# Kernel optimization log

Hardware: AMD Instinct MI355X
Metric: run time of the kernel (lower is better)

## Reference

```python
import jax, jax.numpy as jnp
import numpy as np

EPS = 1e-10


def setup_inputs() -> dict:
    key = jax.random.key(0)
    k1, k2 = jax.random.split(key)
    supports = jax.random.normal(k1, (32, 512, 1024), dtype=jnp.float32)
    targets = jax.random.normal(k2, (32, 512, 1024), dtype=jnp.float32)
    return {"supports": supports, "targets": targets}


def reference(supports, targets):
    # targets: [B, T, D], supports: [B, S, D] -> sim: [B, T, S]
    # F.cosine_similarity(a, b, eps): dot / max(||a||*||b||, eps)
    dots = jnp.einsum("btd,bsd->bts", targets, supports)
    t_norm = jnp.linalg.norm(targets, axis=-1)   # [B, T]
    s_norm = jnp.linalg.norm(supports, axis=-1)  # [B, S]
    denom = jnp.maximum(t_norm[:, :, None] * s_norm[:, None, :], EPS)
    sim = dots / denom
    # normalize=True default: map (-1, 1) -> (0, 1)
    return (sim + 1.0) * 0.5
```

## Files before the change

kernel.cpp:

```cpp
#include <hip/hip_runtime.h>
#include <hip/hip_bf16.h>

typedef __attribute__((ext_vector_type(8))) short short8;
typedef __attribute__((ext_vector_type(4))) float f32x4;

#define NBATCH 32
#define NT 512
#define NS 512
#define ND 1024
#define BM 128
#define BN 128
#define BK 32
#define NK (ND / BK)

__device__ __forceinline__ short f2bf(float f) {
    union { __hip_bfloat16 h; short s; } u;
    u.h = __float2bfloat16(f);
    return u.s;
}

__device__ __forceinline__ short8 cvt8(float4 a, float4 b) {
    short8 r;
    r[0] = f2bf(a.x); r[1] = f2bf(a.y); r[2] = f2bf(a.z); r[3] = f2bf(a.w);
    r[4] = f2bf(b.x); r[5] = f2bf(b.y); r[6] = f2bf(b.z); r[7] = f2bf(b.w);
    return r;
}

__device__ __forceinline__ float ssq4(float s, float4 a) {
    return fmaf(a.x, a.x, fmaf(a.y, a.y, fmaf(a.z, a.z, fmaf(a.w, a.w, s))));
}

__global__ __launch_bounds__(512, 4)
void paircos_mfma(const float* __restrict__ sup, const float* __restrict__ tgt,
                  float* __restrict__ out) {
    __shared__ __align__(16) short As[2][BM * BK];
    __shared__ __align__(16) short Bs[2][BN * BK];
    __shared__ float tn[BM];
    __shared__ float sn[BN];

    const int tid = threadIdx.x;
    const int l    = blockIdx.x;
    const int wgid = (l & 7) * 64 + (l >> 3);
    const int b    = wgid >> 4;
    const int til  = wgid & 15;
    const int bt0  = (til >> 2) * BM;
    const int bs0  = (til & 3) * BN;

    const int seg  = tid & 3;
    const int srow = tid >> 2;

    const float* gA = tgt + (size_t)b * NT * ND + (size_t)(bt0 + srow) * ND + seg * 8;
    const float* gB = sup + (size_t)b * NS * ND + (size_t)(bs0 + srow) * ND + seg * 8;

    const int wave = tid >> 6;
    const int lane = tid & 63;
    const int wr  = (wave >> 2) * 64;
    const int wc  = (wave & 3) * 32;
    const int lhi = lane >> 4;
    const int llo = lane & 15;

    f32x4 acc[4][2];
#pragma unroll
    for (int m = 0; m < 4; ++m)
#pragma unroll
        for (int n = 0; n < 2; ++n)
            acc[m][n] = (f32x4){0.f, 0.f, 0.f, 0.f};

    float sqa = 0.f, sqb = 0.f;

    float4 eA0, eA1, eB0, eB1, oA0, oA1, oB0, oB1;

    const int offw = srow * BK + (((seg + (srow >> 1)) & 3) * 8);

#define LOADT(A0, A1, B0, B1, KK)                                              \
    do {                                                                       \
        A0 = *reinterpret_cast<const float4*>(gA + (KK) * BK);                 \
        A1 = *reinterpret_cast<const float4*>(gA + (KK) * BK + 4);             \
        B0 = *reinterpret_cast<const float4*>(gB + (KK) * BK);                 \
        B1 = *reinterpret_cast<const float4*>(gB + (KK) * BK + 4);             \
    } while (0)

#define STORET(A0, A1, B0, B1, P)                                              \
    do {                                                                       \
        sqa = ssq4(ssq4(sqa, A0), A1);                                         \
        *reinterpret_cast<short8*>(&As[P][offw]) = cvt8(A0, A1);               \
        sqb = ssq4(ssq4(sqb, B0), B1);                                         \
        *reinterpret_cast<short8*>(&Bs[P][offw]) = cvt8(B0, B1);               \
    } while (0)

#define FRAG_READ(P)                                                           \
    do {                                                                       \
        _Pragma("unroll") for (int m = 0; m < 4; ++m) {                        \
            const int row = wr + m * 16 + llo;                                 \
            const int off = row * BK + (((lhi + (row >> 1)) & 3) * 8);         \
            af[m] = *reinterpret_cast<const short8*>(&As[P][off]);             \
        }                                                                      \
        _Pragma("unroll") for (int n = 0; n < 2; ++n) {                        \
            const int row = wc + n * 16 + llo;                                 \
            const int off = row * BK + (((lhi + (row >> 1)) & 3) * 8);         \
            bfr[n] = *reinterpret_cast<const short8*>(&Bs[P][off]);            \
        }                                                                      \
    } while (0)

#define MFMA_BLOCK()                                                           \
    do {                                                                       \
        __builtin_amdgcn_s_setprio(1);                                         \
        _Pragma("unroll") for (int m = 0; m < 4; ++m)                          \
            _Pragma("unroll") for (int n = 0; n < 2; ++n)                      \
                acc[m][n] = __builtin_amdgcn_mfma_f32_16x16x32_bf16(           \
                    af[m], bfr[n], acc[m][n], 0, 0, 0);                        \
        __builtin_amdgcn_s_setprio(0);                                         \
    } while (0)

#define PHASE_FENCE()                                                          \
    do {                                                                       \
        asm volatile("s_waitcnt lgkmcnt(0)" ::: "memory");                     \
        __builtin_amdgcn_s_barrier();                                          \
        asm volatile("" ::: "memory");                                         \
    } while (0)

    LOADT(eA0, eA1, eB0, eB1, 0);
    STORET(eA0, eA1, eB0, eB1, 0);
    LOADT(eA0, eA1, eB0, eB1, 1);
    LOADT(oA0, oA1, oB0, oB1, 2);
    PHASE_FENCE();

    for (int k = 0; k < NK; k += 2) {
        {
            short8 af[4], bfr[2];
            FRAG_READ(0);
            STORET(eA0, eA1, eB0, eB1, 1);
            if (k + 3 < NK) LOADT(eA0, eA1, eB0, eB1, k + 3);
            MFMA_BLOCK();
            PHASE_FENCE();
        }
        {
            short8 af[4], bfr[2];
            FRAG_READ(1);
            if (k + 2 < NK) STORET(oA0, oA1, oB0, oB1, 0);
            if (k + 4 < NK) LOADT(oA0, oA1, oB0, oB1, k + 4);
            MFMA_BLOCK();
            PHASE_FENCE();
        }
    }

    sqa += __shfl_xor(sqa, 1);
    sqa += __shfl_xor(sqa, 2);
    sqb += __shfl_xor(sqb, 1);
    sqb += __shfl_xor(sqb, 2);
    if (seg == 0) {
        tn[srow] = sqrtf(sqa);
        sn[srow] = sqrtf(sqb);
    }
    __syncthreads();

    float* outp = out + (size_t)b * NT * NS;
#pragma unroll
    for (int m = 0; m < 4; ++m) {
        const int lr0 = wr + m * 16 + lhi * 4;
#pragma unroll
        for (int n = 0; n < 2; ++n) {
            const int lc = wc + n * 16 + llo;
            const float snv = sn[lc];
            const int col = bs0 + lc;
#pragma unroll
            for (int j = 0; j < 4; ++j) {
                const float denom = fmaxf(tn[lr0 + j] * snv, 1e-10f);
                outp[(size_t)(bt0 + lr0 + j) * NS + col] =
                    acc[m][n][j] / denom * 0.5f + 0.5f;
            }
        }
    }
}

extern "C" void kernel_launch(void* const* d_in, const int* in_sizes, int n_in,
                              void* d_out, int out_size, void* d_ws, size_t ws_size,
                              hipStream_t stream) {
    const float* sup = (const float*)d_in[0];
    const float* tgt = (const float*)d_in[1];
    float* out = (float*)d_out;
    (void)in_sizes; (void)n_in; (void)out_size; (void)d_ws; (void)ws_size;
    paircos_mfma<<<dim3(16 * NBATCH), 512, 0, stream>>>(sup, tgt, out);
}
```

Measured before the change: 39.30 us.

## Double K tile to 64 with XOR LDS swizzle and fewer barriers

Raises the K tile from 32 to 64 so each barrier-separated phase does two MFMA blocks, halving the number of LDS barriers per output tile. Each thread now loads two rows (row and row+64) with 8 segments per row. The LDS layout switches to an XOR swizzle to avoid bank conflicts, and the prefetch depth drops from two tiles in registers to one. This doubles the LDS footprint and changes the register pressure and latency-hiding balance.

```diff
diff --git a/kernel.cpp b/kernel.cpp
--- a/kernel.cpp
+++ b/kernel.cpp
@@ -10,7 +10,7 @@
 #define ND 1024
 #define BM 128
 #define BN 128
-#define BK 32
+#define BK 64
 #define NK (ND / BK)
 
 __device__ __forceinline__ short f2bf(float f) {
@@ -46,8 +46,8 @@
     const int bt0  = (til >> 2) * BM;
     const int bs0  = (til & 3) * BN;
 
-    const int seg  = tid & 3;
-    const int srow = tid >> 2;
+    const int seg  = tid & 7;
+    const int srow = tid >> 3;
 
     const float* gA = tgt + (size_t)b * NT * ND + (size_t)(bt0 + srow) * ND + seg * 8;
     const float* gB = sup + (size_t)b * NS * ND + (size_t)(bs0 + srow) * ND + seg * 8;
@@ -66,38 +66,48 @@
         for (int n = 0; n < 2; ++n)
             acc[m][n] = (f32x4){0.f, 0.f, 0.f, 0.f};
 
-    float sqa = 0.f, sqb = 0.f;
+    float sqa0 = 0.f, sqa1 = 0.f, sqb0 = 0.f, sqb1 = 0.f;
 
-    float4 eA0, eA1, eB0, eB1, oA0, oA1, oB0, oB1;
+    float4 pA0, pA1, pA2, pA3, pB0, pB1, pB2, pB3;
 
-    const int offw = srow * BK + (((seg + (srow >> 1)) & 3) * 8);
+    const int pu   = (seg ^ (srow & 7)) * 8;
+    const int offw0 = srow * BK + pu;
+    const int offw1 = (srow + 64) * BK + pu;
 
-#define LOADT(A0, A1, B0, B1, KK)                                              \
+#define LOADT(KK)                                                              \
     do {                                                                       \
-        A0 = *reinterpret_cast<const float4*>(gA + (KK) * BK);                 \
-        A1 = *reinterpret_cast<const float4*>(gA + (KK) * BK + 4);             \
-        B0 = *reinterpret_cast<const float4*>(gB + (KK) * BK);                 \
-        B1 = *reinterpret_cast<const float4*>(gB + (KK) * BK + 4);             \
+        pA0 = *reinterpret_cast<const float4*>(gA + (KK) * BK);                \
+        pA1 = *reinterpret_cast<const float4*>(gA + (KK) * BK + 4);            \
+        pA2 = *reinterpret_cast<const float4*>(gA + (KK) * BK + 64 * ND);      \
+        pA3 = *reinterpret_cast<const float4*>(gA + (KK) * BK + 64 * ND + 4);  \
+        pB0 = *reinterpret_cast<const float4*>(gB + (KK) * BK);                \
+        pB1 = *reinterpret_cast<const float4*>(gB + (KK) * BK + 4);            \
+        pB2 = *reinterpret_cast<const float4*>(gB + (KK) * BK + 64 * ND);      \
+        pB3 = *reinterpret_cast<const float4*>(gB + (KK) * BK + 64 * ND + 4);  \
     } while (0)
 
-#define STORET(A0, A1, B0, B1, P)                                              \
+#define STORET(P)                                                              \
     do {                                                                       \
-        sqa = ssq4(ssq4(sqa, A0), A1);                                         \
-        *reinterpret_cast<short8*>(&As[P][offw]) = cvt8(A0, A1);               \
-        sqb = ssq4(ssq4(sqb, B0), B1);                                         \
-        *reinterpret_cast<short8*>(&Bs[P][offw]) = cvt8(B0, B1);               \
+        sqa0 = ssq4(ssq4(sqa0, pA0), pA1);                                     \
+        *reinterpret_cast<short8*>(&As[P][offw0]) = cvt8(pA0, pA1);            \
+        sqa1 = ssq4(ssq4(sqa1, pA2), pA3);                                     \
+        *reinterpret_cast<short8*>(&As[P][offw1]) = cvt8(pA2, pA3);            \
+        sqb0 = ssq4(ssq4(sqb0, pB0), pB1);                                     \
+        *reinterpret_cast<short8*>(&Bs[P][offw0]) = cvt8(pB0, pB1);            \
+        sqb1 = ssq4(ssq4(sqb1, pB2), pB3);                                     \
+        *reinterpret_cast<short8*>(&Bs[P][offw1]) = cvt8(pB2, pB3);            \
     } while (0)
 
-#define FRAG_READ(P)                                                           \
+#define FRAG_READ(P, KS)                                                       \
     do {                                                                       \
         _Pragma("unroll") for (int m = 0; m < 4; ++m) {                        \
             const int row = wr + m * 16 + llo;                                 \
-            const int off = row * BK + (((lhi + (row >> 1)) & 3) * 8);         \
+            const int off = row * BK + ((((KS) * 4 + lhi) ^ (row & 7)) * 8);   \
             af[m] = *reinterpret_cast<const short8*>(&As[P][off]);             \
         }                                                                      \
         _Pragma("unroll") for (int n = 0; n < 2; ++n) {                        \
             const int row = wc + n * 16 + llo;                                 \
-            const int off = row * BK + (((lhi + (row >> 1)) & 3) * 8);         \
+            const int off = row * BK + ((((KS) * 4 + lhi) ^ (row & 7)) * 8);   \
             bfr[n] = *reinterpret_cast<const short8*>(&Bs[P][off]);            \
         }                                                                      \
     } while (0)
@@ -119,38 +129,35 @@
         asm volatile("" ::: "memory");                                         \
     } while (0)
 
-    LOADT(eA0, eA1, eB0, eB1, 0);
-    STORET(eA0, eA1, eB0, eB1, 0);
-    LOADT(eA0, eA1, eB0, eB1, 1);
-    LOADT(oA0, oA1, oB0, oB1, 2);
+    LOADT(0);
+    STORET(0);
+    LOADT(1);
     PHASE_FENCE();
 
-    for (int k = 0; k < NK; k += 2) {
-        {
-            short8 af[4], bfr[2];
-            FRAG_READ(0);
-            STORET(eA0, eA1, eB0, eB1, 1);
-            if (k + 3 < NK) LOADT(eA0, eA1, eB0, eB1, k + 3);
-            MFMA_BLOCK();
-            PHASE_FENCE();
-        }
-        {
-            short8 af[4], bfr[2];
-            FRAG_READ(1);
-            if (k + 2 < NK) STORET(oA0, oA1, oB0, oB1, 0);
-            if (k + 4 < NK) LOADT(oA0, oA1, oB0, oB1, k + 4);
-            MFMA_BLOCK();
-            PHASE_FENCE();
-        }
+    for (int k = 0; k < NK; ++k) {
+        const int cur = k & 1;
+        short8 af[4], bfr[2];
+        FRAG_READ(cur, 0);
+        if (k + 1 < NK) STORET(cur ^ 1);
+        if (k + 2 < NK) LOADT(k + 2);
+        MFMA_BLOCK();
+        FRAG_READ(cur, 1);
+        MFMA_BLOCK();
+        PHASE_FENCE();
     }
 
-    sqa += __shfl_xor(sqa, 1);
-    sqa += __shfl_xor(sqa, 2);
-    sqb += __shfl_xor(sqb, 1);
-    sqb += __shfl_xor(sqb, 2);
+#pragma unroll
+    for (int d = 1; d < 8; d <<= 1) {
+        sqa0 += __shfl_xor(sqa0, d);
+        sqa1 += __shfl_xor(sqa1, d);
+        sqb0 += __shfl_xor(sqb0, d);
+        sqb1 += __shfl_xor(sqb1, d);
+    }
     if (seg == 0) {
-        tn[srow] = sqrtf(sqa);
-        sn[srow] = sqrtf(sqb);
+        tn[srow]      = sqrtf(sqa0);
+        tn[srow + 64] = sqrtf(sqa1);
+        sn[srow]      = sqrtf(sqb0);
+        sn[srow + 64] = sqrtf(sqb1);
     }
     __syncthreads();
 
```

Result: slower. 40.53 us (+3.1%).

## Triple-buffer LDS tiles and prefetch MFMA fragments one step ahead

Applied to the files above, without the earlier changes.

Replaces the double-buffered LDS scheme with three rotating LDS buffers. Register fragments for the next k-step are read while MFMAs run on the current fragments, so LDS read latency overlaps matrix math. Global prefetch depth drops from two tiles in registers to one. The cost is extra LDS per block and more fragment registers, which may hurt occupancy under the 512x4 launch bounds.

```diff
diff --git a/kernel.cpp b/kernel.cpp
--- a/kernel.cpp
+++ b/kernel.cpp
@@ -12,6 +12,7 @@
 #define BN 128
 #define BK 32
 #define NK (ND / BK)
+#define TSZ (BM * BK)
 
 __device__ __forceinline__ short f2bf(float f) {
     union { __hip_bfloat16 h; short s; } u;
@@ -33,8 +34,8 @@
 __global__ __launch_bounds__(512, 4)
 void paircos_mfma(const float* __restrict__ sup, const float* __restrict__ tgt,
                   float* __restrict__ out) {
-    __shared__ __align__(16) short As[2][BM * BK];
-    __shared__ __align__(16) short Bs[2][BN * BK];
+    __shared__ __align__(16) short As[3 * TSZ];
+    __shared__ __align__(16) short Bs[3 * TSZ];
     __shared__ float tn[BM];
     __shared__ float sn[BN];
 
@@ -68,47 +69,48 @@
 
     float sqa = 0.f, sqb = 0.f;
 
-    float4 eA0, eA1, eB0, eB1, oA0, oA1, oB0, oB1;
+    float4 pA0, pA1, pB0, pB1;
+    short8 xa[4], xb[2], ya[4], yb[2];
 
     const int offw = srow * BK + (((seg + (srow >> 1)) & 3) * 8);
 
-#define LOADT(A0, A1, B0, B1, KK)                                              \
+#define LOADT(KK)                                                              \
     do {                                                                       \
-        A0 = *reinterpret_cast<const float4*>(gA + (KK) * BK);                 \
-        A1 = *reinterpret_cast<const float4*>(gA + (KK) * BK + 4);             \
-        B0 = *reinterpret_cast<const float4*>(gB + (KK) * BK);                 \
-        B1 = *reinterpret_cast<const float4*>(gB + (KK) * BK + 4);             \
+        pA0 = *reinterpret_cast<const float4*>(gA + (KK) * BK);                \
+        pA1 = *reinterpret_cast<const float4*>(gA + (KK) * BK + 4);            \
+        pB0 = *reinterpret_cast<const float4*>(gB + (KK) * BK);                \
+        pB1 = *reinterpret_cast<const float4*>(gB + (KK) * BK + 4);            \
     } while (0)
 
-#define STORET(A0, A1, B0, B1, P)                                              \
+#define STORET(WB)                                                             \
     do {                                                                       \
-        sqa = ssq4(ssq4(sqa, A0), A1);                                         \
-        *reinterpret_cast<short8*>(&As[P][offw]) = cvt8(A0, A1);               \
-        sqb = ssq4(ssq4(sqb, B0), B1);                                         \
-        *reinterpret_cast<short8*>(&Bs[P][offw]) = cvt8(B0, B1);               \
+        sqa = ssq4(ssq4(sqa, pA0), pA1);                                       \
+        *reinterpret_cast<short8*>(&As[(WB) + offw]) = cvt8(pA0, pA1);         \
+        sqb = ssq4(ssq4(sqb, pB0), pB1);                                       \
+        *reinterpret_cast<short8*>(&Bs[(WB) + offw]) = cvt8(pB0, pB1);         \
     } while (0)
 
-#define FRAG_READ(P)                                                           \
+#define FRAG_READ(FA, FB, RB)                                                  \
     do {                                                                       \
         _Pragma("unroll") for (int m = 0; m < 4; ++m) {                        \
             const int row = wr + m * 16 + llo;                                 \
-            const int off = row * BK + (((lhi + (row >> 1)) & 3) * 8);         \
-            af[m] = *reinterpret_cast<const short8*>(&As[P][off]);             \
+            const int off = (RB) + row * BK + (((lhi + (row >> 1)) & 3) * 8);  \
+            FA[m] = *reinterpret_cast<const short8*>(&As[off]);                \
         }                                                                      \
         _Pragma("unroll") for (int n = 0; n < 2; ++n) {                        \
             const int row = wc + n * 16 + llo;                                 \
-            const int off = row * BK + (((lhi + (row >> 1)) & 3) * 8);         \
-            bfr[n] = *reinterpret_cast<const short8*>(&Bs[P][off]);            \
+            const int off = (RB) + row * BK + (((lhi + (row >> 1)) & 3) * 8);  \
+            FB[n] = *reinterpret_cast<const short8*>(&Bs[off]);                \
         }                                                                      \
     } while (0)
 
-#define MFMA_BLOCK()                                                           \
+#define MFMA_BLOCK(FA, FB)                                                     \
     do {                                                                       \
         __builtin_amdgcn_s_setprio(1);                                         \
         _Pragma("unroll") for (int m = 0; m < 4; ++m)                          \
             _Pragma("unroll") for (int n = 0; n < 2; ++n)                      \
                 acc[m][n] = __builtin_amdgcn_mfma_f32_16x16x32_bf16(           \
-                    af[m], bfr[n], acc[m][n], 0, 0, 0);                        \
+                    FA[m], FB[n], acc[m][n], 0, 0, 0);                         \
         __builtin_amdgcn_s_setprio(0);                                         \
     } while (0)
 
@@ -119,29 +121,32 @@
         asm volatile("" ::: "memory");                                         \
     } while (0)
 
-    LOADT(eA0, eA1, eB0, eB1, 0);
-    STORET(eA0, eA1, eB0, eB1, 0);
-    LOADT(eA0, eA1, eB0, eB1, 1);
-    LOADT(oA0, oA1, oB0, oB1, 2);
+#define ROTATE()                                                               \
+    do { int t = cbase; cbase = rbase; rbase = wbase; wbase = t; } while (0)
+
+    LOADT(0);
+    STORET(0);
+    LOADT(1);
     PHASE_FENCE();
+    STORET(TSZ);
+    LOADT(2);
+    FRAG_READ(xa, xb, 0);
+    PHASE_FENCE();
+    int cbase = 0, rbase = TSZ, wbase = 2 * TSZ;
 
     for (int k = 0; k < NK; k += 2) {
-        {
-            short8 af[4], bfr[2];
-            FRAG_READ(0);
-            STORET(eA0, eA1, eB0, eB1, 1);
-            if (k + 3 < NK) LOADT(eA0, eA1, eB0, eB1, k + 3);
-            MFMA_BLOCK();
-            PHASE_FENCE();
-        }
-        {
-            short8 af[4], bfr[2];
-            FRAG_READ(1);
-            if (k + 2 < NK) STORET(oA0, oA1, oB0, oB1, 0);
-            if (k + 4 < NK) LOADT(oA0, oA1, oB0, oB1, k + 4);
-            MFMA_BLOCK();
-            PHASE_FENCE();
-        }
+        if (k + 1 < NK) FRAG_READ(ya, yb, rbase);
+        MFMA_BLOCK(xa, xb);
+        if (k + 2 < NK) STORET(wbase);
+        if (k + 3 < NK) LOADT(k + 3);
+        PHASE_FENCE();
+        ROTATE();
+        if (k + 2 < NK) FRAG_READ(xa, xb, rbase);
+        MFMA_BLOCK(ya, yb);
+        if (k + 3 < NK) STORET(wbase);
+        if (k + 4 < NK) LOADT(k + 4);
+        PHASE_FENCE();
+        ROTATE();
     }
 
     sqa += __shfl_xor(sqa, 1);
```

Result: slower. 40.10 us (+2.0%).
